# Performance work log

Hardware: AMD Instinct MI355X
Metric: run time of the kernel (lower is better)

The kernel has to match this reference:

```python
import itertools
import jax, jax.numpy as jnp
import numpy as np

B, N, D = 128, 1024, 256
G, GSZ, REL_DIM, KD, PD, NF = 64, 3, 16, 64, 64, 64


def sinusoidal_pe(n, d):
    # standard transformer sinusoidal positional encoding, shape (n, d)
    pos = jnp.arange(n, dtype=jnp.float32)[:, None]
    i = jnp.arange(d, dtype=jnp.float32)[None, :]
    angle = pos / jnp.power(10000.0, (2.0 * jnp.floor(i / 2.0)) / d)
    return jnp.where(jnp.arange(d)[None, :] % 2 == 0, jnp.sin(angle), jnp.cos(angle))


def setup_inputs() -> dict:
    key = jax.random.key(0)
    k0, k1, k2, k3, k4, k5 = jax.random.split(key, 6)
    x = jax.random.normal(k0, (B, N, D), jnp.float32)
    # graphlet filter bank (random_normal init)
    filters = 0.05 * jax.random.normal(k1, (NF, GSZ, GSZ, REL_DIM), jnp.float32)
    # learned group queries: Embedding(n_groups*graphlet_size, key_dim)
    query_emb = 0.05 * jax.random.normal(k2, (G * GSZ, KD), jnp.float32)
    # Dense(key_dim, use_bias=False) for attention keys
    Wk_map = jax.random.normal(k3, (D, KD), jnp.float32) / np.sqrt(D)
    # MultiDimInnerProdRelation: per-relation-dim query/key projections
    Wq = jax.random.normal(k4, (REL_DIM, D, PD), jnp.float32) / np.sqrt(D)
    Wk = jax.random.normal(k5, (REL_DIM, D, PD), jnp.float32) / np.sqrt(D)
    return {"x": x, "filters": filters, "query_emb": query_emb,
            "Wk_map": Wk_map, "Wq": Wq, "Wk": Wk}


def reference(x, filters, query_emb, Wk_map, Wq, Wk):
    beta = KD ** (-0.5)
    # group attention: keys = Dense(x) + positional embedding ('pos+feat')
    k = jnp.einsum('bnd,dk->bnk', x, Wk_map) + sinusoidal_pe(N, KD)[None]
    scores = jax.nn.softmax(beta * jnp.einsum('qk,bnk->bqn', query_emb, k), axis=-1)
    gobj = jnp.einsum('bqn,bnd->bqd', scores, x).reshape(B, G, GSZ, D)
    # MultiDimInnerProdRelation within each group: R[b,g,i,j,r] = <Wq_r x_i, Wk_r x_j>
    zq = jnp.einsum('bgnd,rdp->bgrnp', gobj, Wq)
    zk = jnp.einsum('bgmd,rdp->bgrmp', gobj, Wk)
    R = jnp.einsum('bgrnp,bgrmp->bgnmr', zq, zk)  # (B, G, GSZ, GSZ, REL_DIM)
    # symmetric relational inner product: aggregate (mean) over permutations
    perms = jnp.array(list(itertools.permutations(range(GSZ))))  # (P, GSZ)
    Rp = R[:, :, perms[:, :, None], perms[:, None, :], :]  # (B, G, P, GSZ, GSZ, REL_DIM)
    ip = jnp.einsum('bgpnmr,fnmr->bgpf', Rp, filters)
    return jnp.mean(ip, axis=2)  # (B, n_groups, n_filters)
```

## Files before the change

### kernel.cpp

```cpp
#include <hip/hip_runtime.h>
#include <math.h>

#define B_   128
#define N_   1024
#define D_   256
#define G_   64
#define GSZ_ 3
#define RD_  16
#define KD_  64
#define PD_  64
#define NF_  64
#define Q_   (G_*GSZ_)

typedef __attribute__((ext_vector_type(8))) short bf16x8;
typedef __attribute__((ext_vector_type(4))) float f32x4;

__device__ __forceinline__ unsigned short f2bf(float f) {
    unsigned int u = __float_as_uint(f);
    u += 0x7fffu + ((u >> 16) & 1u);
    return (unsigned short)(u >> 16);
}

__global__ void coef_kernel(const float* __restrict__ filters,
                            float* __restrict__ coef) {
    int flat = blockIdx.x * 256 + threadIdx.x;
    if (flat >= NF_ * RD_) return;
    int f = flat >> 4, r = flat & 15;
    const float* F = filters + f * 144 + r;
    float diag = F[0] + F[48 + 16] + F[96 + 32];
    float all = 0.f;
#pragma unroll
    for (int u = 0; u < 3; ++u)
#pragma unroll
        for (int v = 0; v < 3; ++v) all += F[u * 48 + v * 16];
    float a = diag * (1.f / 3.f);
    float b = (all - diag) * (1.f / 6.f);
    coef[f * 16 + r] = a - b;
    coef[1024 + f * 16 + r] = b;
}

__global__ void wb_kernel(const float* __restrict__ Wq,
                          const float* __restrict__ Wk,
                          unsigned short* __restrict__ Wb) {
    int flat = blockIdx.x * 256 + threadIdx.x;
    int d = flat & 255, col = flat >> 8;
    int ch = col & 1023;
    const float* W = (col >> 10) ? Wk : Wq;
    float v = W[((size_t)(ch >> 6) * 256 + d) * 64 + (ch & 63)];
    Wb[(size_t)col * 256 + d] = f2bf(v);
}

__global__ void qeb_kernel(const float* __restrict__ qe,
                           unsigned short* __restrict__ qeb) {
    int i = blockIdx.x * 256 + threadIdx.x;
    if (i < Q_ * KD_) qeb[i] = f2bf(qe[i] * 0.125f);
}

__global__ void wkt_kernel(const float* __restrict__ Wk_map,
                           unsigned short* __restrict__ WkTb) {
    int i = blockIdx.x * 256 + threadIdx.x;
    int kd = i >> 8, d = i & 255;
    WkTb[kd * 256 + d] = f2bf(Wk_map[d * 64 + kd]);
}

__global__ __launch_bounds__(256)
void xt_kernel(const float* __restrict__ x,
               unsigned short* __restrict__ xTb) {
    __shared__ float xs[128][65];
    int b = blockIdx.z, d0 = blockIdx.y * 64, n0 = blockIdx.x * 128;
    int t = threadIdx.x;
#pragma unroll
    for (int i = 0; i < 8; ++i) {
        int f = i * 256 + t;
        int row = f >> 4, c4 = f & 15;
        float4 v = *(const float4*)(x + ((size_t)b * N_ + n0 + row) * D_ + d0 + c4 * 4);
        xs[row][c4 * 4 + 0] = v.x; xs[row][c4 * 4 + 1] = v.y;
        xs[row][c4 * 4 + 2] = v.z; xs[row][c4 * 4 + 3] = v.w;
    }
    __syncthreads();
#pragma unroll
    for (int i = 0; i < 4; ++i) {
        int f = i * 256 + t;
        int dr = f >> 4, seg = f & 15;
        uint4 uv;
        unsigned int* up = (unsigned int*)&uv;
#pragma unroll
        for (int j = 0; j < 4; ++j) {
            unsigned int lo = f2bf(xs[seg * 8 + 2 * j][dr]);
            unsigned int hi = f2bf(xs[seg * 8 + 2 * j + 1][dr]);
            up[j] = lo | (hi << 16);
        }
        *(uint4*)(xTb + ((size_t)b * D_ + d0 + dr) * N_ + n0 + seg * 8) = uv;
    }
}

#define WKP 264

__global__ __launch_bounds__(256, 2)
void kproj2_kernel(const float* __restrict__ x,
                   const unsigned short* __restrict__ WkTb,
                   unsigned short* __restrict__ kb) {
    __shared__ unsigned short wkts[64 * WKP];
    __shared__ unsigned short xs[64 * WKP];
    __shared__ unsigned short Ks[64 * 72];
    int b = blockIdx.y, n0 = blockIdx.x * 64;
    int t = threadIdx.x, w = t >> 6, lane = t & 63;
    int quad = lane >> 4, lcol = lane & 15;

#pragma unroll
    for (int i = 0; i < 8; ++i) {
        int f = i * 256 + t;
        int row = f >> 5, seg = f & 31;
        *(uint4*)(&wkts[row * WKP + seg * 8]) = *(const uint4*)(WkTb + row * 256 + seg * 8);
    }
#pragma unroll
    for (int i = 0; i < 16; ++i) {
        int f = i * 256 + t;
        int row = f >> 6, c4 = f & 63;
        float4 v = *(const float4*)(x + ((size_t)b * N_ + n0 + row) * D_ + c4 * 4);
        uint2 uv;
        uv.x = (unsigned int)f2bf(v.x) | ((unsigned int)f2bf(v.y) << 16);
        uv.y = (unsigned int)f2bf(v.z) | ((unsigned int)f2bf(v.w) << 16);
        *(uint2*)(&xs[row * WKP + c4 * 4]) = uv;
    }
    __syncthreads();

    f32x4 z[4];
#pragma unroll
    for (int mt = 0; mt < 4; ++mt) z[mt] = (f32x4)(0.f);
#pragma unroll
    for (int kk = 0; kk < 8; ++kk) {
        bf16x8 bf = *(const bf16x8*)(&xs[(w * 16 + lcol) * WKP + kk * 32 + quad * 8]);
#pragma unroll
        for (int mt = 0; mt < 4; ++mt) {
            bf16x8 af = *(const bf16x8*)(&wkts[(mt * 16 + lcol) * WKP + kk * 32 + quad * 8]);
            z[mt] = __builtin_amdgcn_mfma_f32_16x16x32_bf16(af, bf, z[mt], 0, 0, 0);
        }
    }

    int nl = w * 16 + lcol;
    int n = n0 + nl;
#pragma unroll
    for (int mt = 0; mt < 4; ++mt)
#pragma unroll
        for (int r = 0; r < 4; ++r) {
            int kd = mt * 16 + quad * 4 + r;
            float freq  = expf(-(float)(kd >> 1) * (logf(10000.0f) / 32.0f));
            float angle = (float)n * freq;
            float pe    = (kd & 1) ? cosf(angle) : sinf(angle);
            Ks[nl * 72 + kd] = f2bf(z[mt][r] + pe);
        }
    __syncthreads();

#pragma unroll
    for (int i = 0; i < 2; ++i) {
        int f = i * 256 + t;
        int row = f >> 3, seg = f & 7;
        *(uint4*)(kb + ((size_t)b * N_ + n0 + row) * KD_ + seg * 8) =
            *(const uint4*)(&Ks[row * 72 + seg * 8]);
    }
}

#define KBP 72
#define XTP 72
#define PSP 72

__global__ __launch_bounds__(256, 2)
void attn2_kernel(const unsigned short* __restrict__ qeb,
                  const unsigned short* __restrict__ kb,
                  const unsigned short* __restrict__ xTb,
                  unsigned short* __restrict__ gobj) {
    __shared__ unsigned short kbs[64 * KBP];
    __shared__ unsigned short xts[256 * XTP];
    __shared__ unsigned short ps [96 * PSP];
    __shared__ float Rs[96][4];
    __shared__ float invs[96];

    int b = blockIdx.x >> 1, qh = blockIdx.x & 1;
    int t = threadIdx.x, w = t >> 6, lane = t & 63;
    int quad = lane >> 4, lcol = lane & 15;
    int q0 = qh * 96;

    bf16x8 qef[6][2];
#pragma unroll
    for (int mt = 0; mt < 6; ++mt)
#pragma unroll
        for (int ks = 0; ks < 2; ++ks)
            qef[mt][ks] = *(const bf16x8*)(qeb + (q0 + mt * 16 + lcol) * KD_ + ks * 32 + quad * 8);

    f32x4 acc[4][6];
#pragma unroll
    for (int i = 0; i < 4; ++i)
#pragma unroll
        for (int mt = 0; mt < 6; ++mt) acc[i][mt] = (f32x4)(0.f);
    float rsum[6][4];
#pragma unroll
    for (int mt = 0; mt < 6; ++mt)
#pragma unroll
        for (int r = 0; r < 4; ++r) rsum[mt][r] = 0.f;

    const unsigned short* kbB = kb + (size_t)b * N_ * KD_;
    const unsigned short* xtB = xTb + (size_t)b * D_ * N_;

    for (int c = 0; c < 16; ++c) {
        __syncthreads();
#pragma unroll
        for (int i = 0; i < 2; ++i) {
            int flat = i * 256 + t;
            int row = flat >> 3, seg = flat & 7;
            *(uint4*)(kbs + row * KBP + seg * 8) =
                *(const uint4*)(kbB + (size_t)(c * 64 + row) * KD_ + seg * 8);
        }
#pragma unroll
        for (int i = 0; i < 8; ++i) {
            int flat = i * 256 + t;
            int row = flat >> 3, seg = flat & 7;
            *(uint4*)(xts + row * XTP + seg * 8) =
                *(const uint4*)(xtB + (size_t)row * N_ + c * 64 + seg * 8);
        }
        __syncthreads();

        f32x4 s[6];
#pragma unroll
        for (int mt = 0; mt < 6; ++mt) s[mt] = (f32x4)(0.f);
#pragma unroll
        for (int ks = 0; ks < 2; ++ks) {
            bf16x8 bf = *(const bf16x8*)(kbs + (w * 16 + lcol) * KBP + ks * 32 + quad * 8);
#pragma unroll
            for (int mt = 0; mt < 6; ++mt)
                s[mt] = __builtin_amdgcn_mfma_f32_16x16x32_bf16(qef[mt][ks], bf, s[mt], 0, 0, 0);
        }
#pragma unroll
        for (int mt = 0; mt < 6; ++mt)
#pragma unroll
            for (int r = 0; r < 4; ++r) {
                float e = __expf(s[mt][r]);
                rsum[mt][r] += e;
                ps[(mt * 16 + quad * 4 + r) * PSP + w * 16 + lcol] = f2bf(e);
            }
        __syncthreads();

#pragma unroll
        for (int ks = 0; ks < 2; ++ks) {
            bf16x8 af[6];
#pragma unroll
            for (int mt = 0; mt < 6; ++mt)
                af[mt] = *(const bf16x8*)(ps + (mt * 16 + lcol) * PSP + ks * 32 + quad * 8);
#pragma unroll
            for (int i = 0; i < 4; ++i) {
                int dt = i * 4 + w;
                bf16x8 bf = *(const bf16x8*)(xts + (dt * 16 + lcol) * XTP + ks * 32 + quad * 8);
#pragma unroll
                for (int mt = 0; mt < 6; ++mt)
                    acc[i][mt] = __builtin_amdgcn_mfma_f32_16x16x32_bf16(af[mt], bf, acc[i][mt], 0, 0, 0);
            }
        }
    }

#pragma unroll
    for (int mt = 0; mt < 6; ++mt)
#pragma unroll
        for (int r = 0; r < 4; ++r) {
            float v = rsum[mt][r];
            v += __shfl_xor(v, 1, 64);
            v += __shfl_xor(v, 2, 64);
            v += __shfl_xor(v, 4, 64);
            v += __shfl_xor(v, 8, 64);
            rsum[mt][r] = v;
        }
    if (lcol == 0) {
#pragma unroll
        for (int mt = 0; mt < 6; ++mt)
#pragma unroll
            for (int r = 0; r < 4; ++r)
                Rs[mt * 16 + quad * 4 + r][w] = rsum[mt][r];
    }
    __syncthreads();
    if (t < 96) invs[t] = 1.0f / (Rs[t][0] + Rs[t][1] + Rs[t][2] + Rs[t][3]);
    __syncthreads();

    unsigned short* gB = gobj + ((size_t)b * Q_ + q0) * D_;
#pragma unroll
    for (int i = 0; i < 4; ++i) {
        int dt = i * 4 + w;
#pragma unroll
        for (int mt = 0; mt < 6; ++mt)
#pragma unroll
            for (int r = 0; r < 4; ++r) {
                int q = mt * 16 + quad * 4 + r;
                gB[q * D_ + dt * 16 + lcol] = f2bf(acc[i][mt][r] * invs[q]);
            }
    }
}

#define APITCH 264

__global__ __launch_bounds__(256, 2)
void rel2_kernel(const unsigned short* __restrict__ gobj,
                 const unsigned short* __restrict__ Wb,
                 const float* __restrict__ coef,
                 float* __restrict__ out) {
    __shared__ unsigned short As[64 * APITCH];
    __shared__ unsigned short Ws[64 * APITCH];
    __shared__ float Tp[4 * 16 * 2 * 16];

    int t = threadIdx.x;
    int w = t >> 6, lane = t & 63;
    int quad = lane >> 4, lcol = lane & 15;
    int bg0 = blockIdx.x * 16;

    for (int i = 0; i < 8; ++i) {
        int idx = i * 256 + t;
        int r3 = idx >> 7, c3 = idx & 127;
        ((unsigned int*)As)[(r3 * 4 + 3) * (APITCH / 2) + c3] = 0u;
    }
#pragma unroll
    for (int it = 0; it < 6; ++it) {
        int flat = it * 256 + t;
        int j = flat >> 5, seg = flat & 31;
        *(uint4*)(&As[((j / 3) * 4 + (j % 3)) * APITCH + seg * 8]) =
            *(const uint4*)(gobj + ((size_t)(bg0 * 3 + j)) * D_ + seg * 8);
    }

    f32x4 zq[4], zk[4];
    for (int r = 0; r < 16; ++r) {
#pragma unroll
        for (int half = 0; half < 2; ++half) {
            __syncthreads();
            const unsigned short* src = Wb + (size_t)(r + half * 16) * 64 * 256;
#pragma unroll
            for (int it = 0; it < 8; ++it) {
                int flat = it * 256 + t;
                int col = flat >> 5, ch = flat & 31;
                uint4 v = *(const uint4*)(src + col * 256 + ch * 8);
                *(uint4*)(&Ws[col * APITCH + ch * 8]) = v;
            }
            __syncthreads();

            f32x4* z = half ? zk : zq;
#pragma unroll
            for (int i = 0; i < 4; ++i) z[i] = (f32x4)(0.f);
#pragma unroll
            for (int kk = 0; kk < 8; ++kk) {
                bf16x8 bfrag = *(const bf16x8*)(&Ws[(w * 16 + lcol) * APITCH + kk * 32 + quad * 8]);
#pragma unroll
                for (int mt = 0; mt < 4; ++mt) {
                    bf16x8 afrag = *(const bf16x8*)(&As[(mt * 16 + lcol) * APITCH + kk * 32 + quad * 8]);
                    z[mt] = __builtin_amdgcn_mfma_f32_16x16x32_bf16(afrag, bfrag, z[mt], 0, 0, 0);
                }
            }
        }
#pragma unroll
        for (int mt = 0; mt < 4; ++mt) {
            float t1 = zq[mt].x * zk[mt].x + zq[mt].y * zk[mt].y +
                       zq[mt].z * zk[mt].z + zq[mt].w * zk[mt].w;
            float sq = zq[mt].x + zq[mt].y + zq[mt].z + zq[mt].w;
            float sk = zk[mt].x + zk[mt].y + zk[mt].z + zk[mt].w;
            float t2 = sq * sk;
#pragma unroll
            for (int off = 1; off < 16; off <<= 1) {
                t1 += __shfl_xor(t1, off, 64);
                t2 += __shfl_xor(t2, off, 64);
            }
            if (lcol == 0) {
                int bgl = mt * 4 + quad;
                Tp[((w * 16 + bgl) * 2 + 0) * 16 + r] = t1;
                Tp[((w * 16 + bgl) * 2 + 1) * 16 + r] = t2;
            }
        }
    }
    __syncthreads();

    int f = t & 63;
#pragma unroll
    for (int i = 0; i < 4; ++i) {
        int bgl = w * 4 + i;
        float acc = 0.f;
#pragma unroll
        for (int r = 0; r < 16; ++r) {
            float T1 = Tp[((0 * 16 + bgl) * 2 + 0) * 16 + r] + Tp[((1 * 16 + bgl) * 2 + 0) * 16 + r] +
                       Tp[((2 * 16 + bgl) * 2 + 0) * 16 + r] + Tp[((3 * 16 + bgl) * 2 + 0) * 16 + r];
            float T2 = Tp[((0 * 16 + bgl) * 2 + 1) * 16 + r] + Tp[((1 * 16 + bgl) * 2 + 1) * 16 + r] +
                       Tp[((2 * 16 + bgl) * 2 + 1) * 16 + r] + Tp[((3 * 16 + bgl) * 2 + 1) * 16 + r];
            acc += coef[f * 16 + r] * T1 + coef[1024 + f * 16 + r] * T2;
        }
        out[(size_t)(bg0 + bgl) * NF_ + f] = acc;
    }
}

extern "C" void kernel_launch(void* const* d_in, const int* in_sizes, int n_in,
                              void* d_out, int out_size, void* d_ws, size_t ws_size,
                              hipStream_t stream) {
    const float* x         = (const float*)d_in[0];
    const float* filters   = (const float*)d_in[1];
    const float* query_emb = (const float*)d_in[2];
    const float* Wk_map    = (const float*)d_in[3];
    const float* Wq        = (const float*)d_in[4];
    const float* Wk        = (const float*)d_in[5];
    float* out = (float*)d_out;

    char* p = (char*)d_ws;
    unsigned short* xTb  = (unsigned short*)p;  p += (size_t)B_*D_*N_*2;
    unsigned short* kbp  = (unsigned short*)p;  p += (size_t)B_*N_*KD_*2;
    unsigned short* gobj = (unsigned short*)p;  p += (size_t)B_*Q_*D_*2;
    unsigned short* Wb   = (unsigned short*)p;  p += (size_t)2048*256*2;
    float*          coef = (float*)p;           p += 2048*4;
    unsigned short* qeb  = (unsigned short*)p;  p += (size_t)Q_*KD_*2;
    unsigned short* WkTb = (unsigned short*)p;  p += (size_t)KD_*D_*2;

    hipLaunchKernelGGL(wkt_kernel, dim3(64), dim3(256), 0, stream,
                       Wk_map, WkTb);
    hipLaunchKernelGGL(xt_kernel, dim3(8, 4, 128), dim3(256), 0, stream,
                       x, xTb);
    hipLaunchKernelGGL(kproj2_kernel, dim3(16, 128), dim3(256), 0, stream,
                       x, WkTb, kbp);
    hipLaunchKernelGGL(qeb_kernel, dim3(48), dim3(256), 0, stream,
                       query_emb, qeb);
    hipLaunchKernelGGL(coef_kernel, dim3(4), dim3(256), 0, stream,
                       filters, coef);
    hipLaunchKernelGGL(wb_kernel, dim3(2048), dim3(256), 0, stream,
                       Wq, Wk, Wb);
    hipLaunchKernelGGL(attn2_kernel, dim3(256), dim3(256), 0, stream,
                       qeb, kbp, xTb, gobj);
    hipLaunchKernelGGL(rel2_kernel, dim3(512), dim3(256), 0, stream,
                       gobj, Wb, coef, out);
}
```

Baseline: 401.6 us.

## Read attention and relation operands directly from global memory and widen attention blocks

After: 358.4 us. 10.8% less time.

```diff
diff --git a/kernel.cpp b/kernel.cpp
--- a/kernel.cpp
+++ b/kernel.cpp
@@ -39,15 +39,32 @@
     coef[1024 + f * 16 + r] = b;
 }
 
-__global__ void wb_kernel(const float* __restrict__ Wq,
-                          const float* __restrict__ Wk,
-                          unsigned short* __restrict__ Wb) {
-    int flat = blockIdx.x * 256 + threadIdx.x;
-    int d = flat & 255, col = flat >> 8;
-    int ch = col & 1023;
-    const float* W = (col >> 10) ? Wk : Wq;
-    float v = W[((size_t)(ch >> 6) * 256 + d) * 64 + (ch & 63)];
-    Wb[(size_t)col * 256 + d] = f2bf(v);
+__global__ __launch_bounds__(256)
+void wb2_kernel(const float* __restrict__ Wq,
+                const float* __restrict__ Wk,
+                unsigned short* __restrict__ Wb) {
+    __shared__ unsigned short wt[64 * 264];
+    int qk = blockIdx.x >> 4, r = blockIdx.x & 15;
+    const float* W = qk ? Wk : Wq;
+    int t = threadIdx.x;
+#pragma unroll
+    for (int i = 0; i < 16; ++i) {
+        int flat = i * 256 + t;
+        int d = flat >> 4, p4 = flat & 15;
+        float4 v = *(const float4*)(W + ((size_t)r * 256 + d) * 64 + p4 * 4);
+        wt[(p4 * 4 + 0) * 264 + d] = f2bf(v.x);
+        wt[(p4 * 4 + 1) * 264 + d] = f2bf(v.y);
+        wt[(p4 * 4 + 2) * 264 + d] = f2bf(v.z);
+        wt[(p4 * 4 + 3) * 264 + d] = f2bf(v.w);
+    }
+    __syncthreads();
+#pragma unroll
+    for (int i = 0; i < 8; ++i) {
+        int flat = i * 256 + t;
+        int p = flat >> 5, seg = flat & 31;
+        *(uint4*)(Wb + ((size_t)(qk * 1024 + r * 64 + p)) * 256 + seg * 8) =
+            *(const uint4*)(&wt[p * 264 + seg * 8]);
+    }
 }
 
 __global__ void qeb_kernel(const float* __restrict__ qe,
@@ -161,19 +178,15 @@
     }
 }
 
-#define KBP 72
-#define XTP 72
-#define PSP 72
-
-__global__ __launch_bounds__(256, 2)
-void attn2_kernel(const unsigned short* __restrict__ qeb,
+#define PSP2 136
+
+__global__ __launch_bounds__(512, 2)
+void attn4_kernel(const unsigned short* __restrict__ qeb,
                   const unsigned short* __restrict__ kb,
                   const unsigned short* __restrict__ xTb,
                   unsigned short* __restrict__ gobj) {
-    __shared__ unsigned short kbs[64 * KBP];
-    __shared__ unsigned short xts[256 * XTP];
-    __shared__ unsigned short ps [96 * PSP];
-    __shared__ float Rs[96][4];
+    __shared__ unsigned short ps[96 * PSP2];
+    __shared__ float Rs[96][8];
     __shared__ float invs[96];
 
     int b = blockIdx.x >> 1, qh = blockIdx.x & 1;
@@ -188,9 +201,9 @@
         for (int ks = 0; ks < 2; ++ks)
             qef[mt][ks] = *(const bf16x8*)(qeb + (q0 + mt * 16 + lcol) * KD_ + ks * 32 + quad * 8);
 
-    f32x4 acc[4][6];
-#pragma unroll
-    for (int i = 0; i < 4; ++i)
+    f32x4 acc[2][6];
+#pragma unroll
+    for (int i = 0; i < 2; ++i)
 #pragma unroll
         for (int mt = 0; mt < 6; ++mt) acc[i][mt] = (f32x4)(0.f);
     float rsum[6][4];
@@ -202,30 +215,13 @@
     const unsigned short* kbB = kb + (size_t)b * N_ * KD_;
     const unsigned short* xtB = xTb + (size_t)b * D_ * N_;
 
-    for (int c = 0; c < 16; ++c) {
-        __syncthreads();
-#pragma unroll
-        for (int i = 0; i < 2; ++i) {
-            int flat = i * 256 + t;
-            int row = flat >> 3, seg = flat & 7;
-            *(uint4*)(kbs + row * KBP + seg * 8) =
-                *(const uint4*)(kbB + (size_t)(c * 64 + row) * KD_ + seg * 8);
-        }
-#pragma unroll
-        for (int i = 0; i < 8; ++i) {
-            int flat = i * 256 + t;
-            int row = flat >> 3, seg = flat & 7;
-            *(uint4*)(xts + row * XTP + seg * 8) =
-                *(const uint4*)(xtB + (size_t)row * N_ + c * 64 + seg * 8);
-        }
-        __syncthreads();
-
+    for (int c = 0; c < 8; ++c) {
         f32x4 s[6];
 #pragma unroll
         for (int mt = 0; mt < 6; ++mt) s[mt] = (f32x4)(0.f);
 #pragma unroll
         for (int ks = 0; ks < 2; ++ks) {
-            bf16x8 bf = *(const bf16x8*)(kbs + (w * 16 + lcol) * KBP + ks * 32 + quad * 8);
+            bf16x8 bf = *(const bf16x8*)(kbB + (size_t)(c * 128 + w * 16 + lcol) * KD_ + ks * 32 + quad * 8);
 #pragma unroll
             for (int mt = 0; mt < 6; ++mt)
                 s[mt] = __builtin_amdgcn_mfma_f32_16x16x32_bf16(qef[mt][ks], bf, s[mt], 0, 0, 0);
@@ -235,21 +231,27 @@
 #pragma unroll
             for (int r = 0; r < 4; ++r) {
                 float e = __expf(s[mt][r]);
+                s[mt][r] = e;
                 rsum[mt][r] += e;
-                ps[(mt * 16 + quad * 4 + r) * PSP + w * 16 + lcol] = f2bf(e);
             }
         __syncthreads();
-
-#pragma unroll
-        for (int ks = 0; ks < 2; ++ks) {
+#pragma unroll
+        for (int mt = 0; mt < 6; ++mt)
+#pragma unroll
+            for (int r = 0; r < 4; ++r)
+                ps[(mt * 16 + quad * 4 + r) * PSP2 + w * 16 + lcol] = f2bf(s[mt][r]);
+        __syncthreads();
+
+#pragma unroll
+        for (int ks = 0; ks < 4; ++ks) {
             bf16x8 af[6];
 #pragma unroll
             for (int mt = 0; mt < 6; ++mt)
-                af[mt] = *(const bf16x8*)(ps + (mt * 16 + lcol) * PSP + ks * 32 + quad * 8);
-#pragma unroll
-            for (int i = 0; i < 4; ++i) {
-                int dt = i * 4 + w;
-                bf16x8 bf = *(const bf16x8*)(xts + (dt * 16 + lcol) * XTP + ks * 32 + quad * 8);
+                af[mt] = *(const bf16x8*)(ps + (mt * 16 + lcol) * PSP2 + ks * 32 + quad * 8);
+#pragma unroll
+            for (int i = 0; i < 2; ++i) {
+                int dt = i * 8 + w;
+                bf16x8 bf = *(const bf16x8*)(xtB + (size_t)(dt * 16 + lcol) * N_ + c * 128 + ks * 32 + quad * 8);
 #pragma unroll
                 for (int mt = 0; mt < 6; ++mt)
                     acc[i][mt] = __builtin_amdgcn_mfma_f32_16x16x32_bf16(af[mt], bf, acc[i][mt], 0, 0, 0);
@@ -276,13 +278,18 @@
                 Rs[mt * 16 + quad * 4 + r][w] = rsum[mt][r];
     }
     __syncthreads();
-    if (t < 96) invs[t] = 1.0f / (Rs[t][0] + Rs[t][1] + Rs[t][2] + Rs[t][3]);
+    if (t < 96) {
+        float s8 = 0.f;
+#pragma unroll
+        for (int ww = 0; ww < 8; ++ww) s8 += Rs[t][ww];
+        invs[t] = 1.0f / s8;
+    }
     __syncthreads();
 
     unsigned short* gB = gobj + ((size_t)b * Q_ + q0) * D_;
 #pragma unroll
-    for (int i = 0; i < 4; ++i) {
-        int dt = i * 4 + w;
+    for (int i = 0; i < 2; ++i) {
+        int dt = i * 8 + w;
 #pragma unroll
         for (int mt = 0; mt < 6; ++mt)
 #pragma unroll
@@ -293,61 +300,59 @@
     }
 }
 
-#define APITCH 264
+#define AP4 264
 
 __global__ __launch_bounds__(256, 2)
-void rel2_kernel(const unsigned short* __restrict__ gobj,
+void rel4_kernel(const unsigned short* __restrict__ gobj,
                  const unsigned short* __restrict__ Wb,
                  const float* __restrict__ coef,
                  float* __restrict__ out) {
-    __shared__ unsigned short As[64 * APITCH];
-    __shared__ unsigned short Ws[64 * APITCH];
-    __shared__ float Tp[4 * 16 * 2 * 16];
-
-    int t = threadIdx.x;
-    int w = t >> 6, lane = t & 63;
+    __shared__ unsigned short As[64 * AP4];
+    __shared__ float Tp[2048];
+
+    int t = threadIdx.x, w = t >> 6, lane = t & 63;
     int quad = lane >> 4, lcol = lane & 15;
     int bg0 = blockIdx.x * 16;
-
-    for (int i = 0; i < 8; ++i) {
+    int pcol = w * 16 + lcol;
+
+#pragma unroll
+    for (int i = 0; i < 2; ++i) {
         int idx = i * 256 + t;
-        int r3 = idx >> 7, c3 = idx & 127;
-        ((unsigned int*)As)[(r3 * 4 + 3) * (APITCH / 2) + c3] = 0u;
-    }
-#pragma unroll
-    for (int it = 0; it < 6; ++it) {
-        int flat = it * 256 + t;
-        int j = flat >> 5, seg = flat & 31;
-        *(uint4*)(&As[((j / 3) * 4 + (j % 3)) * APITCH + seg * 8]) =
-            *(const uint4*)(gobj + ((size_t)(bg0 * 3 + j)) * D_ + seg * 8);
-    }
-
-    f32x4 zq[4], zk[4];
+        int r3 = idx >> 5, c4 = idx & 31;
+        uint4 zz; zz.x = zz.y = zz.z = zz.w = 0u;
+        *(uint4*)(&As[(r3 * 4 + 3) * AP4 + c4 * 8]) = zz;
+    }
+#pragma unroll
+    for (int i = 0; i < 6; ++i) {
+        int idx = i * 256 + t;
+        int j = idx >> 5, c4 = idx & 31;
+        *(uint4*)(&As[((j / 3) * 4 + (j % 3)) * AP4 + c4 * 8]) =
+            *(const uint4*)(gobj + ((size_t)(bg0 * 3 + j)) * 256 + c4 * 8);
+    }
+    __syncthreads();
+
+    bf16x8 af[4][8];
+#pragma unroll
+    for (int mt = 0; mt < 4; ++mt)
+#pragma unroll
+        for (int kk = 0; kk < 8; ++kk)
+            af[mt][kk] = *(const bf16x8*)(&As[(mt * 16 + lcol) * AP4 + kk * 32 + quad * 8]);
+
     for (int r = 0; r < 16; ++r) {
-#pragma unroll
-        for (int half = 0; half < 2; ++half) {
-            __syncthreads();
-            const unsigned short* src = Wb + (size_t)(r + half * 16) * 64 * 256;
-#pragma unroll
-            for (int it = 0; it < 8; ++it) {
-                int flat = it * 256 + t;
-                int col = flat >> 5, ch = flat & 31;
-                uint4 v = *(const uint4*)(src + col * 256 + ch * 8);
-                *(uint4*)(&Ws[col * APITCH + ch * 8]) = v;
-            }
-            __syncthreads();
-
-            f32x4* z = half ? zk : zq;
-#pragma unroll
-            for (int i = 0; i < 4; ++i) z[i] = (f32x4)(0.f);
-#pragma unroll
-            for (int kk = 0; kk < 8; ++kk) {
-                bf16x8 bfrag = *(const bf16x8*)(&Ws[(w * 16 + lcol) * APITCH + kk * 32 + quad * 8]);
-#pragma unroll
-                for (int mt = 0; mt < 4; ++mt) {
-                    bf16x8 afrag = *(const bf16x8*)(&As[(mt * 16 + lcol) * APITCH + kk * 32 + quad * 8]);
-                    z[mt] = __builtin_amdgcn_mfma_f32_16x16x32_bf16(afrag, bfrag, z[mt], 0, 0, 0);
-                }
+        f32x4 zq[4], zk[4];
+#pragma unroll
+        for (int mt = 0; mt < 4; ++mt) { zq[mt] = (f32x4)(0.f); zk[mt] = (f32x4)(0.f); }
+        const unsigned short* bqp = Wb + (size_t)(r * 64 + pcol) * 256;
+        const unsigned short* bkp = bqp + (size_t)1024 * 256;
+#pragma unroll
+        for (int kk = 0; kk < 8; ++kk) {
+            int co = kk * 32 + quad * 8;
+            bf16x8 bq = *(const bf16x8*)(bqp + co);
+            bf16x8 bk = *(const bf16x8*)(bkp + co);
+#pragma unroll
+            for (int mt = 0; mt < 4; ++mt) {
+                zq[mt] = __builtin_amdgcn_mfma_f32_16x16x32_bf16(af[mt][kk], bq, zq[mt], 0, 0, 0);
+                zk[mt] = __builtin_amdgcn_mfma_f32_16x16x32_bf16(af[mt][kk], bk, zk[mt], 0, 0, 0);
             }
         }
 #pragma unroll
@@ -371,20 +376,20 @@
     }
     __syncthreads();
 
-    int f = t & 63;
+    int f = t & 63, grp = t >> 6;
 #pragma unroll
     for (int i = 0; i < 4; ++i) {
-        int bgl = w * 4 + i;
-        float acc = 0.f;
+        int bgl = grp * 4 + i;
+        float a = 0.f;
 #pragma unroll
         for (int r = 0; r < 16; ++r) {
             float T1 = Tp[((0 * 16 + bgl) * 2 + 0) * 16 + r] + Tp[((1 * 16 + bgl) * 2 + 0) * 16 + r] +
                        Tp[((2 * 16 + bgl) * 2 + 0) * 16 + r] + Tp[((3 * 16 + bgl) * 2 + 0) * 16 + r];
             float T2 = Tp[((0 * 16 + bgl) * 2 + 1) * 16 + r] + Tp[((1 * 16 + bgl) * 2 + 1) * 16 + r] +
                        Tp[((2 * 16 + bgl) * 2 + 1) * 16 + r] + Tp[((3 * 16 + bgl) * 2 + 1) * 16 + r];
-            acc += coef[f * 16 + r] * T1 + coef[1024 + f * 16 + r] * T2;
-        }
-        out[(size_t)(bg0 + bgl) * NF_ + f] = acc;
+            a += coef[f * 16 + r] * T1 + coef[1024 + f * 16 + r] * T2;
+        }
+        out[(size_t)(bg0 + bgl) * NF_ + f] = a;
     }
 }
 
@@ -418,10 +423,10 @@
                        query_emb, qeb);
     hipLaunchKernelGGL(coef_kernel, dim3(4), dim3(256), 0, stream,
                        filters, coef);
-    hipLaunchKernelGGL(wb_kernel, dim3(2048), dim3(256), 0, stream,
+    hipLaunchKernelGGL(wb2_kernel, dim3(32), dim3(256), 0, stream,
                        Wq, Wk, Wb);
-    hipLaunchKernelGGL(attn2_kernel, dim3(256), dim3(256), 0, stream,
+    hipLaunchKernelGGL(attn4_kernel, dim3(256), dim3(512), 0, stream,
                        qeb, kbp, xTb, gobj);
-    hipLaunchKernelGGL(rel2_kernel, dim3(512), dim3(256), 0, stream,
+    hipLaunchKernelGGL(rel4_kernel, dim3(512), dim3(256), 0, stream,
                        gobj, Wb, coef, out);
 }
```
